# Optimization experiments

Measured on AMD Instinct MI355X. Metric: run time of the kernel, lower is better.

Reference implementation:

```python
import jax, jax.numpy as jnp
import numpy as np

TOP_K = 2


def setup_inputs() -> dict:
    key = jax.random.key(0)
    k1, k2 = jax.random.split(key)
    x = jax.random.normal(k1, (4, 4096, 2048), dtype=jnp.float32)
    W = jax.random.normal(k2, (64, 2048), dtype=jnp.float32) * (1.0 / np.sqrt(2048))
    return {"x": x, "W": W}


def reference(x, W):
    B, S, D = x.shape
    E = W.shape[0]
    # logits: [B*S, E] via linear router (no bias)
    flat = x.reshape(-1, D)
    logits = jnp.einsum('td,ed->te', flat, W)
    probs = jax.nn.softmax(logits, axis=-1)
    # eval path: top-k indices
    _, top_k_indices = jax.lax.top_k(probs, TOP_K)          # [T, K]
    # scatter 1s -> mask; scatter gathered probs -> router_probs (== probs*mask)
    router_mask = jax.nn.one_hot(top_k_indices, E, dtype=probs.dtype).sum(axis=-2)  # [T, E]
    router_probs = probs * router_mask
    # normalize (top_k > 1: gradient flows through the sum)
    router_probs = router_probs / router_probs.sum(axis=-1, keepdims=True)
    return (router_mask.reshape(B, S, E),
            top_k_indices.reshape(B, S, TOP_K),
            router_probs.reshape(B, S, E),
            probs.reshape(B, S, E))
```

## Files before the change

kernel.cpp:

```cpp
#include <hip/hip_runtime.h>
#include <math.h>


#define D_DIM 2048
#define E_DIM 64
#define NCH   (D_DIM >> 6)

typedef __bf16 bf16x8 __attribute__((ext_vector_type(8)));
typedef unsigned short us8 __attribute__((ext_vector_type(8)));
typedef float f32x4 __attribute__((ext_vector_type(4)));

static __device__ __forceinline__ unsigned short f2bf(float f) {
    unsigned int u = __float_as_uint(f);
    u += 0x7fffu + ((u >> 16) & 1u);
    return (unsigned short)(u >> 16);
}
static __device__ __forceinline__ float bf2f(unsigned short h) {
    return __uint_as_float(((unsigned int)h) << 16);
}
static __device__ __forceinline__ void split4(const float4 v, ushort4* h, ushort4* l) {
    h->x = f2bf(v.x); l->x = f2bf(v.x - bf2f(h->x));
    h->y = f2bf(v.y); l->y = f2bf(v.y - bf2f(h->y));
    h->z = f2bf(v.z); l->z = f2bf(v.z - bf2f(h->z));
    h->w = f2bf(v.w); l->w = f2bf(v.w - bf2f(h->w));
}

static __device__ __forceinline__ void gld_lds16(const void* g, void* l) {
    __builtin_amdgcn_global_load_lds(
        (const __attribute__((address_space(1))) unsigned int*)g,
        (__attribute__((address_space(3))) unsigned int*)l,
        16, 0, 0);
}

__global__ __launch_bounds__(256, 1) void convert_w(
    const float4* __restrict__ W4, unsigned short* __restrict__ WH,
    unsigned short* __restrict__ WL)
{
    int i = blockIdx.x * 256 + threadIdx.x;
    float4 v = W4[i];
    ushort4 h, l;
    split4(v, &h, &l);
    *(ushort4*)&WH[i * 4] = h;
    *(ushort4*)&WL[i * 4] = l;
}

__global__ __launch_bounds__(256, 4) void router_fused(
    const float* __restrict__ x,
    const unsigned short* __restrict__ WHg, const unsigned short* __restrict__ WLg,
    float* __restrict__ mask_out, float* __restrict__ idx_out,
    float* __restrict__ rp_out, float* __restrict__ probs_out)
{
    __shared__ __align__(16) unsigned short XH [2][16 * 64];
    __shared__ __align__(16) unsigned short XL [2][16 * 64];
    __shared__ __align__(16) unsigned short WHs[2][64 * 64];
    __shared__ __align__(16) unsigned short WLs[2][64 * 64];

    const int tid  = threadIdx.x;
    const int lane = tid & 63;
    const int wv   = tid >> 6;
    const int quad = lane >> 4;
    const int l16  = lane & 15;

    const int t0 = blockIdx.x << 4;

    f32x4 acc = {0.f, 0.f, 0.f, 0.f};

    const int we = wv * 8 + (lane >> 3);
    const int wo = lane & 7;

    const float* xg = x + (size_t)(t0 + l16) * D_DIM + wv * 16 + quad * 4;

    const int g   = wv * 4 + quad;
    const int cwb = l16 * 128 + (((g >> 1) ^ (l16 & 7)) << 4) + (g & 1) * 8;

    float4 xc = *(const float4*)(xg);
    #pragma unroll
    for (int i2 = 0; i2 < 2; ++i2) {
        int e  = i2 * 32 + we;
        int og = wo ^ (e & 7);
        gld_lds16(WHg + (size_t)e * D_DIM + og * 8, &WHs[0][(i2 * 256 + wv * 64) * 8]);
        gld_lds16(WLg + (size_t)e * D_DIM + og * 8, &WLs[0][(i2 * 256 + wv * 64) * 8]);
    }

    for (int ch = 0; ch < NCH; ++ch) {
        const int b = ch & 1;

        float4 xn;
        if (ch + 1 < NCH) xn = *(const float4*)(xg + (ch + 1) * 64);

        {
            ushort4 h, l;
            split4(xc, &h, &l);
            *(ushort4*)((char*)&XH[b][0] + cwb) = h;
            *(ushort4*)((char*)&XL[b][0] + cwb) = l;
        }

        if (ch + 1 < NCH) asm volatile("s_waitcnt vmcnt(1)" ::: "memory");
        else              asm volatile("s_waitcnt vmcnt(0)" ::: "memory");
        asm volatile("s_waitcnt lgkmcnt(0)" ::: "memory");
        __builtin_amdgcn_sched_barrier(0);
        __builtin_amdgcn_s_barrier();
        __builtin_amdgcn_sched_barrier(0);

        if (ch + 1 < NCH) {
            const int kc = (ch + 1) << 6;
            const int nb = b ^ 1;
            #pragma unroll
            for (int i2 = 0; i2 < 2; ++i2) {
                int e  = i2 * 32 + we;
                int og = wo ^ (e & 7);
                gld_lds16(WHg + (size_t)e * D_DIM + kc + og * 8,
                          &WHs[nb][(i2 * 256 + wv * 64) * 8]);
                gld_lds16(WLg + (size_t)e * D_DIM + kc + og * 8,
                          &WLs[nb][(i2 * 256 + wv * 64) * 8]);
            }
        }

        #pragma unroll
        for (int ks = 0; ks < 2; ++ks) {
            const int sr = ks * 4 + quad;
            const int ab = l16 * 128 + ((sr ^ (l16 & 7)) << 4);
            bf16x8 ah = *(const bf16x8*)((const char*)&XH[b][0] + ab);
            bf16x8 al = *(const bf16x8*)((const char*)&XL[b][0] + ab);

            const int e = wv * 16 + l16;
            const int o = ks * 4 + quad;
            const int s = e * 8 + (o ^ (e & 7));
            bf16x8 bh = *(const bf16x8*)&WHs[b][s * 8];
            bf16x8 bl = *(const bf16x8*)&WLs[b][s * 8];
            acc = __builtin_amdgcn_mfma_f32_16x16x32_bf16(ah, bh, acc, 0, 0, 0);
            acc = __builtin_amdgcn_mfma_f32_16x16x32_bf16(al, bh, acc, 0, 0, 0);
            acc = __builtin_amdgcn_mfma_f32_16x16x32_bf16(ah, bl, acc, 0, 0, 0);
        }

        if (ch + 1 < NCH) xc = xn;
    }

    float* L = (float*)&WHs[0][0];
    #pragma unroll
    for (int r = 0; r < 4; ++r)
        L[(quad * 4 + r) * 64 + wv * 16 + l16] = acc[r];
    __syncthreads();

    for (int i = 0; i < 4; ++i) {
        const int tl = wv * 4 + i;
        const int t  = t0 + tl;
        const float v = L[tl * 64 + lane];

        float bv = v; int bi = lane;
        #pragma unroll
        for (int off = 1; off < 64; off <<= 1) {
            float ov = __shfl_xor(bv, off, 64);
            int   oi = __shfl_xor(bi, off, 64);
            bool take = (ov > bv) || (ov == bv && oi < bi);
            bv = take ? ov : bv;
            bi = take ? oi : bi;
        }
        const float m = bv; const int i1 = bi;

        const float p = __expf(v - m);
        float s = p;
        #pragma unroll
        for (int off = 1; off < 64; off <<= 1) s += __shfl_xor(s, off, 64);
        const float prob = p / s;

        const float v2 = (lane == i1) ? -INFINITY : v;
        float cv = v2; int ci = lane;
        #pragma unroll
        for (int off = 1; off < 64; off <<= 1) {
            float ov = __shfl_xor(cv, off, 64);
            int   oi = __shfl_xor(ci, off, 64);
            bool take = (ov > cv) || (ov == cv && oi < ci);
            cv = take ? ov : cv;
            ci = take ? oi : ci;
        }
        const int i2 = ci;

        const float pd = __shfl(prob, i1, 64) + __shfl(prob, i2, 64);
        const bool top = (lane == i1) || (lane == i2);

        const size_t base = (size_t)t * 64 + lane;
        mask_out[base]  = top ? 1.f : 0.f;
        rp_out[base]    = top ? prob / pd : 0.f;
        probs_out[base] = prob;
        if (lane == 0) {
            idx_out[(size_t)t * 2]     = (float)i1;
            idx_out[(size_t)t * 2 + 1] = (float)i2;
        }
    }
}

extern "C" void kernel_launch(void* const* d_in, const int* in_sizes, int n_in,
                              void* d_out, int out_size, void* d_ws, size_t ws_size,
                              hipStream_t stream) {
    const float* x = (const float*)d_in[0];
    const float* W = (const float*)d_in[1];
    float* out = (float*)d_out;

    const int T  = in_sizes[0] / D_DIM;
    const int WN = in_sizes[1];

    unsigned short* WH = (unsigned short*)d_ws;
    unsigned short* WL = WH + WN;

    float* mask_out  = out;
    float* idx_out   = out + (size_t)T * E_DIM;
    float* rp_out    = idx_out + (size_t)T * 2;
    float* probs_out = rp_out + (size_t)T * E_DIM;

    convert_w<<<dim3(WN / 1024), dim3(256), 0, stream>>>((const float4*)W, WH, WL);
    router_fused<<<dim3(T / 16), dim3(256), 0, stream>>>(
        x, WH, WL, mask_out, idx_out, rp_out, probs_out);
}
```

Before: 218.3 us.

## Load W fragments directly into registers and double-buffer across unrolled chunks

The W hi/lo bf16 tiles are no longer staged through LDS with global_load_lds. Each lane now loads its MFMA B-operand fragments straight from global memory into registers. The K loop is unrolled by two, with register double buffering of both W fragments and the next x vectors, so loads for the next chunk are issued before the current chunk's MFMAs. This removes the LDS writes and reads for W and the vmcnt waits, and cuts shared memory to the x tiles only. The trade-off is more registers and uncoalesced per-lane 16-byte global loads of W that rely on L2 hits.

```diff
diff --git a/kernel.cpp b/kernel.cpp
--- a/kernel.cpp
+++ b/kernel.cpp
@@ -7,7 +7,6 @@
 #define NCH   (D_DIM >> 6)
 
 typedef __bf16 bf16x8 __attribute__((ext_vector_type(8)));
-typedef unsigned short us8 __attribute__((ext_vector_type(8)));
 typedef float f32x4 __attribute__((ext_vector_type(4)));
 
 static __device__ __forceinline__ unsigned short f2bf(float f) {
@@ -23,13 +22,6 @@
     h->y = f2bf(v.y); l->y = f2bf(v.y - bf2f(h->y));
     h->z = f2bf(v.z); l->z = f2bf(v.z - bf2f(h->z));
     h->w = f2bf(v.w); l->w = f2bf(v.w - bf2f(h->w));
-}
-
-static __device__ __forceinline__ void gld_lds16(const void* g, void* l) {
-    __builtin_amdgcn_global_load_lds(
-        (const __attribute__((address_space(1))) unsigned int*)g,
-        (__attribute__((address_space(3))) unsigned int*)l,
-        16, 0, 0);
 }
 
 __global__ __launch_bounds__(256, 1) void convert_w(
@@ -44,16 +36,24 @@
     *(ushort4*)&WL[i * 4] = l;
 }
 
+struct WR { bf16x8 h0, h1, l0, l1; };
+
+static __device__ __forceinline__ void ldwr(
+    WR& w, const unsigned short* ph, const unsigned short* pl, int q8) {
+    w.h0 = *(const bf16x8*)(ph + q8);
+    w.h1 = *(const bf16x8*)(ph + 32 + q8);
+    w.l0 = *(const bf16x8*)(pl + q8);
+    w.l1 = *(const bf16x8*)(pl + 32 + q8);
+}
+
 __global__ __launch_bounds__(256, 4) void router_fused(
     const float* __restrict__ x,
     const unsigned short* __restrict__ WHg, const unsigned short* __restrict__ WLg,
     float* __restrict__ mask_out, float* __restrict__ idx_out,
     float* __restrict__ rp_out, float* __restrict__ probs_out)
 {
-    __shared__ __align__(16) unsigned short XH [2][16 * 64];
-    __shared__ __align__(16) unsigned short XL [2][16 * 64];
-    __shared__ __align__(16) unsigned short WHs[2][64 * 64];
-    __shared__ __align__(16) unsigned short WLs[2][64 * 64];
+    __shared__ __align__(16) unsigned short XH[2][16 * 64];
+    __shared__ __align__(16) unsigned short XL[2][16 * 64];
 
     const int tid  = threadIdx.x;
     const int lane = tid & 63;
@@ -65,78 +65,77 @@
 
     f32x4 acc = {0.f, 0.f, 0.f, 0.f};
 
-    const int we = wv * 8 + (lane >> 3);
-    const int wo = lane & 7;
-
     const float* xg = x + (size_t)(t0 + l16) * D_DIM + wv * 16 + quad * 4;
-
     const int g   = wv * 4 + quad;
     const int cwb = l16 * 128 + (((g >> 1) ^ (l16 & 7)) << 4) + (g & 1) * 8;
 
-    float4 xc = *(const float4*)(xg);
-    #pragma unroll
-    for (int i2 = 0; i2 < 2; ++i2) {
-        int e  = i2 * 32 + we;
-        int og = wo ^ (e & 7);
-        gld_lds16(WHg + (size_t)e * D_DIM + og * 8, &WHs[0][(i2 * 256 + wv * 64) * 8]);
-        gld_lds16(WLg + (size_t)e * D_DIM + og * 8, &WLs[0][(i2 * 256 + wv * 64) * 8]);
+    const int e = wv * 16 + l16;
+    const unsigned short* whp = WHg + (size_t)e * D_DIM;
+    const unsigned short* wlp = WLg + (size_t)e * D_DIM;
+    const int q8 = quad * 8;
+
+    const int ab0 = l16 * 128 + ((( quad     ) ^ (l16 & 7)) << 4);
+    const int ab1 = l16 * 128 + (((4 + quad  ) ^ (l16 & 7)) << 4);
+
+#define CONVERT_WRITE(xv, b) do {                                  \
+        ushort4 _h, _l;                                            \
+        split4((xv), &_h, &_l);                                    \
+        *(ushort4*)((char*)&XH[(b)][0] + cwb) = _h;                \
+        *(ushort4*)((char*)&XL[(b)][0] + cwb) = _l;                \
+    } while (0)
+
+#define COMPUTE(b, w) do {                                                     \
+        bf16x8 _ah0 = *(const bf16x8*)((const char*)&XH[(b)][0] + ab0);        \
+        bf16x8 _al0 = *(const bf16x8*)((const char*)&XL[(b)][0] + ab0);        \
+        acc = __builtin_amdgcn_mfma_f32_16x16x32_bf16(_ah0, (w).h0, acc, 0,0,0);\
+        acc = __builtin_amdgcn_mfma_f32_16x16x32_bf16(_al0, (w).h0, acc, 0,0,0);\
+        acc = __builtin_amdgcn_mfma_f32_16x16x32_bf16(_ah0, (w).l0, acc, 0,0,0);\
+        bf16x8 _ah1 = *(const bf16x8*)((const char*)&XH[(b)][0] + ab1);        \
+        bf16x8 _al1 = *(const bf16x8*)((const char*)&XL[(b)][0] + ab1);        \
+        acc = __builtin_amdgcn_mfma_f32_16x16x32_bf16(_ah1, (w).h1, acc, 0,0,0);\
+        acc = __builtin_amdgcn_mfma_f32_16x16x32_bf16(_al1, (w).h1, acc, 0,0,0);\
+        acc = __builtin_amdgcn_mfma_f32_16x16x32_bf16(_ah1, (w).l1, acc, 0,0,0);\
+    } while (0)
+
+#define PUBLISH() do {                                   \
+        asm volatile("s_waitcnt lgkmcnt(0)" ::: "memory");\
+        __builtin_amdgcn_sched_barrier(0);               \
+        __builtin_amdgcn_s_barrier();                    \
+        __builtin_amdgcn_sched_barrier(0);               \
+    } while (0)
+
+    WR wA, wB;
+    float4 xa, xb;
+
+    {
+        float4 x0v = *(const float4*)(xg);
+        ldwr(wA, whp, wlp, q8);
+        xa = *(const float4*)(xg + 64);
+        CONVERT_WRITE(x0v, 0);
+        PUBLISH();
     }
 
-    for (int ch = 0; ch < NCH; ++ch) {
-        const int b = ch & 1;
-
-        float4 xn;
-        if (ch + 1 < NCH) xn = *(const float4*)(xg + (ch + 1) * 64);
-
-        {
-            ushort4 h, l;
-            split4(xc, &h, &l);
-            *(ushort4*)((char*)&XH[b][0] + cwb) = h;
-            *(ushort4*)((char*)&XL[b][0] + cwb) = l;
-        }
-
-        if (ch + 1 < NCH) asm volatile("s_waitcnt vmcnt(1)" ::: "memory");
-        else              asm volatile("s_waitcnt vmcnt(0)" ::: "memory");
-        asm volatile("s_waitcnt lgkmcnt(0)" ::: "memory");
-        __builtin_amdgcn_sched_barrier(0);
-        __builtin_amdgcn_s_barrier();
-        __builtin_amdgcn_sched_barrier(0);
-
+    for (int ch = 0; ch < NCH; ch += 2) {
+        if (ch + 2 < NCH) xb = *(const float4*)(xg + (ch + 2) * 64);
+        if (ch + 1 < NCH) ldwr(wB, whp + (ch + 1) * 64, wlp + (ch + 1) * 64, q8);
+        COMPUTE(ch & 1, wA);
         if (ch + 1 < NCH) {
-            const int kc = (ch + 1) << 6;
-            const int nb = b ^ 1;
-            #pragma unroll
-            for (int i2 = 0; i2 < 2; ++i2) {
-                int e  = i2 * 32 + we;
-                int og = wo ^ (e & 7);
-                gld_lds16(WHg + (size_t)e * D_DIM + kc + og * 8,
-                          &WHs[nb][(i2 * 256 + wv * 64) * 8]);
-                gld_lds16(WLg + (size_t)e * D_DIM + kc + og * 8,
-                          &WLs[nb][(i2 * 256 + wv * 64) * 8]);
-            }
-        }
-
-        #pragma unroll
-        for (int ks = 0; ks < 2; ++ks) {
-            const int sr = ks * 4 + quad;
-            const int ab = l16 * 128 + ((sr ^ (l16 & 7)) << 4);
-            bf16x8 ah = *(const bf16x8*)((const char*)&XH[b][0] + ab);
-            bf16x8 al = *(const bf16x8*)((const char*)&XL[b][0] + ab);
-
-            const int e = wv * 16 + l16;
-            const int o = ks * 4 + quad;
-            const int s = e * 8 + (o ^ (e & 7));
-            bf16x8 bh = *(const bf16x8*)&WHs[b][s * 8];
-            bf16x8 bl = *(const bf16x8*)&WLs[b][s * 8];
-            acc = __builtin_amdgcn_mfma_f32_16x16x32_bf16(ah, bh, acc, 0, 0, 0);
-            acc = __builtin_amdgcn_mfma_f32_16x16x32_bf16(al, bh, acc, 0, 0, 0);
-            acc = __builtin_amdgcn_mfma_f32_16x16x32_bf16(ah, bl, acc, 0, 0, 0);
-        }
-
-        if (ch + 1 < NCH) xc = xn;
+            CONVERT_WRITE(xa, (ch + 1) & 1);
+            PUBLISH();
+        }
+
+        const int co = ch + 1;
+        if (co + 2 < NCH) xa = *(const float4*)(xg + (co + 2) * 64);
+        if (co + 1 < NCH) ldwr(wA, whp + (co + 1) * 64, wlp + (co + 1) * 64, q8);
+        COMPUTE(co & 1, wB);
+        if (co + 1 < NCH) {
+            CONVERT_WRITE(xb, (co + 1) & 1);
+            PUBLISH();
+        }
     }
 
-    float* L = (float*)&WHs[0][0];
+    __syncthreads();
+    float* L = (float*)&XH[0][0];
     #pragma unroll
     for (int r = 0; r < 4; ++r)
         L[(quad * 4 + r) * 64 + wv * 16 + l16] = acc[r];
@@ -188,6 +187,9 @@
             idx_out[(size_t)t * 2 + 1] = (float)i2;
         }
     }
+#undef CONVERT_WRITE
+#undef COMPUTE
+#undef PUBLISH
 }
 
 extern "C" void kernel_launch(void* const* d_in, const int* in_sizes, int n_in,
```

Result: slower. 239.0 us (+9.5%).

## Stream raw fp32 x into LDS via async loads and double tile to 32 tokens

Applied to the files above, without the earlier changes.

X tiles are now loaded straight into LDS as fp32 with global_load_lds, using a 4-deep ring buffer, instead of going through registers and being split into bf16 hi/lo before storing. The split now happens after the LDS read, inside the compute loop. Each block handles 32 tokens instead of 16, so every W chunk loaded is reused across twice as many tokens, and the pipeline runs several chunks ahead. The costs are more LDS, a lower occupancy bound (launch_bounds 2 instead of 4), half as many blocks, and split arithmetic repeated by each wave in the compute path.

```diff
diff --git a/kernel.cpp b/kernel.cpp
--- a/kernel.cpp
+++ b/kernel.cpp
@@ -44,14 +44,13 @@
     *(ushort4*)&WL[i * 4] = l;
 }
 
-__global__ __launch_bounds__(256, 4) void router_fused(
+__global__ __launch_bounds__(256, 2) void router_fused(
     const float* __restrict__ x,
     const unsigned short* __restrict__ WHg, const unsigned short* __restrict__ WLg,
     float* __restrict__ mask_out, float* __restrict__ idx_out,
     float* __restrict__ rp_out, float* __restrict__ probs_out)
 {
-    __shared__ __align__(16) unsigned short XH [2][16 * 64];
-    __shared__ __align__(16) unsigned short XL [2][16 * 64];
+    __shared__ __align__(16) float          XF [4][32 * 64];
     __shared__ __align__(16) unsigned short WHs[2][64 * 64];
     __shared__ __align__(16) unsigned short WLs[2][64 * 64];
 
@@ -61,89 +60,114 @@
     const int quad = lane >> 4;
     const int l16  = lane & 15;
 
-    const int t0 = blockIdx.x << 4;
-
-    f32x4 acc = {0.f, 0.f, 0.f, 0.f};
-
-    const int we = wv * 8 + (lane >> 3);
-    const int wo = lane & 7;
-
-    const float* xg = x + (size_t)(t0 + l16) * D_DIM + wv * 16 + quad * 4;
-
-    const int g   = wv * 4 + quad;
-    const int cwb = l16 * 128 + (((g >> 1) ^ (l16 & 7)) << 4) + (g & 1) * 8;
-
-    float4 xc = *(const float4*)(xg);
+    const int t0 = blockIdx.x << 5;
+
+    f32x4 acc[2];
+    {
+        f32x4 z = {0.f, 0.f, 0.f, 0.f};
+        acc[0] = z; acc[1] = z;
+    }
+
+    const int xr0 = wv * 4 + (lane >> 4);
+    const int xc  = (lane & 15) ^ (xr0 & 15);
+    const int we0 = wv * 8 + (lane >> 3);
+    const int wo  = (lane & 7) ^ (we0 & 7);
+
+    const int e  = wv * 16 + l16;
+    const int e8 = e * 8;
+    const int ek = e & 7;
+
+#define STAGE_X(cc, xi) do {                                                   \
+        const int _kc = (cc) << 6;                                             \
+        gld_lds16(x + (size_t)(t0 + xr0) * D_DIM + _kc + xc * 4,               \
+                  &XF[xi][(wv * 64) * 4]);                                     \
+        gld_lds16(x + (size_t)(t0 + 16 + xr0) * D_DIM + _kc + xc * 4,          \
+                  &XF[xi][(256 + wv * 64) * 4]);                               \
+    } while (0)
+
+#define STAGE_W(cc, wi) do {                                                   \
+        const int _kc = (cc) << 6;                                             \
+        gld_lds16(WHg + (size_t)we0 * D_DIM + _kc + wo * 8,                    \
+                  &WHs[wi][(wv * 64) * 8]);                                    \
+        gld_lds16(WHg + (size_t)(32 + we0) * D_DIM + _kc + wo * 8,             \
+                  &WHs[wi][(256 + wv * 64) * 8]);                              \
+        gld_lds16(WLg + (size_t)we0 * D_DIM + _kc + wo * 8,                    \
+                  &WLs[wi][(wv * 64) * 8]);                                    \
+        gld_lds16(WLg + (size_t)(32 + we0) * D_DIM + _kc + wo * 8,             \
+                  &WLs[wi][(256 + wv * 64) * 8]);                              \
+    } while (0)
+
+#define COMPUTE(wb_, xb_) do {                                                 \
+        _Pragma("unroll")                                                      \
+        for (int ks = 0; ks < 2; ++ks) {                                       \
+            const int o  = ks * 4 + quad;                                      \
+            const int sW = e8 + (o ^ ek);                                      \
+            bf16x8 bh = *(const bf16x8*)&WHs[wb_][sW * 8];                     \
+            bf16x8 bl = *(const bf16x8*)&WLs[wb_][sW * 8];                     \
+            _Pragma("unroll")                                                  \
+            for (int th = 0; th < 2; ++th) {                                   \
+                const int tr = th * 16 + l16;                                  \
+                const int c0 = ks * 8 + quad * 2;                              \
+                float4 va = *(const float4*)                                   \
+                    &XF[xb_][(tr * 16 + ( c0      ^ l16)) * 4];                \
+                float4 vb = *(const float4*)                                   \
+                    &XF[xb_][(tr * 16 + ((c0 + 1) ^ l16)) * 4];                \
+                ushort4 h0, l0, h1, l1;                                        \
+                split4(va, &h0, &l0);                                          \
+                split4(vb, &h1, &l1);                                          \
+                union { us8 u; bf16x8 b; } ua, ul;                             \
+                ua.u = (us8){h0.x, h0.y, h0.z, h0.w, h1.x, h1.y, h1.z, h1.w};  \
+                ul.u = (us8){l0.x, l0.y, l0.z, l0.w, l1.x, l1.y, l1.z, l1.w};  \
+                acc[th] = __builtin_amdgcn_mfma_f32_16x16x32_bf16(             \
+                    ua.b, bh, acc[th], 0, 0, 0);                               \
+                acc[th] = __builtin_amdgcn_mfma_f32_16x16x32_bf16(             \
+                    ul.b, bh, acc[th], 0, 0, 0);                               \
+                acc[th] = __builtin_amdgcn_mfma_f32_16x16x32_bf16(             \
+                    ua.b, bl, acc[th], 0, 0, 0);                               \
+            }                                                                  \
+        }                                                                      \
+    } while (0)
+
+#define BARX() do {                                                            \
+        __builtin_amdgcn_sched_barrier(0);                                     \
+        __builtin_amdgcn_s_barrier();                                          \
+        __builtin_amdgcn_sched_barrier(0);                                     \
+    } while (0)
+
+    STAGE_X(0, 0);
+    STAGE_X(1, 1);
+    STAGE_W(0, 0);
+    STAGE_X(2, 2);
+
+    for (int ch = 0; ch <= 28; ++ch) {
+        asm volatile("s_waitcnt vmcnt(1)" ::: "memory");
+        BARX();
+        STAGE_W(ch + 1, (ch + 1) & 1);
+        STAGE_X(ch + 3, (ch + 3) & 3);
+        COMPUTE(ch & 1, ch & 3);
+    }
+    asm volatile("s_waitcnt vmcnt(1)" ::: "memory");
+    BARX();
+    STAGE_W(30, 0);
+    COMPUTE(1, 1);
+    asm volatile("s_waitcnt vmcnt(0)" ::: "memory");
+    BARX();
+    STAGE_W(31, 1);
+    COMPUTE(0, 2);
+    asm volatile("s_waitcnt vmcnt(0)" ::: "memory");
+    BARX();
+    COMPUTE(1, 3);
+
+    float* L = (float*)&XF[0][0];
     #pragma unroll
-    for (int i2 = 0; i2 < 2; ++i2) {
-        int e  = i2 * 32 + we;
-        int og = wo ^ (e & 7);
-        gld_lds16(WHg + (size_t)e * D_DIM + og * 8, &WHs[0][(i2 * 256 + wv * 64) * 8]);
-        gld_lds16(WLg + (size_t)e * D_DIM + og * 8, &WLs[0][(i2 * 256 + wv * 64) * 8]);
-    }
-
-    for (int ch = 0; ch < NCH; ++ch) {
-        const int b = ch & 1;
-
-        float4 xn;
-        if (ch + 1 < NCH) xn = *(const float4*)(xg + (ch + 1) * 64);
-
-        {
-            ushort4 h, l;
-            split4(xc, &h, &l);
-            *(ushort4*)((char*)&XH[b][0] + cwb) = h;
-            *(ushort4*)((char*)&XL[b][0] + cwb) = l;
-        }
-
-        if (ch + 1 < NCH) asm volatile("s_waitcnt vmcnt(1)" ::: "memory");
-        else              asm volatile("s_waitcnt vmcnt(0)" ::: "memory");
-        asm volatile("s_waitcnt lgkmcnt(0)" ::: "memory");
-        __builtin_amdgcn_sched_barrier(0);
-        __builtin_amdgcn_s_barrier();
-        __builtin_amdgcn_sched_barrier(0);
-
-        if (ch + 1 < NCH) {
-            const int kc = (ch + 1) << 6;
-            const int nb = b ^ 1;
-            #pragma unroll
-            for (int i2 = 0; i2 < 2; ++i2) {
-                int e  = i2 * 32 + we;
-                int og = wo ^ (e & 7);
-                gld_lds16(WHg + (size_t)e * D_DIM + kc + og * 8,
-                          &WHs[nb][(i2 * 256 + wv * 64) * 8]);
-                gld_lds16(WLg + (size_t)e * D_DIM + kc + og * 8,
-                          &WLs[nb][(i2 * 256 + wv * 64) * 8]);
-            }
-        }
-
-        #pragma unroll
-        for (int ks = 0; ks < 2; ++ks) {
-            const int sr = ks * 4 + quad;
-            const int ab = l16 * 128 + ((sr ^ (l16 & 7)) << 4);
-            bf16x8 ah = *(const bf16x8*)((const char*)&XH[b][0] + ab);
-            bf16x8 al = *(const bf16x8*)((const char*)&XL[b][0] + ab);
-
-            const int e = wv * 16 + l16;
-            const int o = ks * 4 + quad;
-            const int s = e * 8 + (o ^ (e & 7));
-            bf16x8 bh = *(const bf16x8*)&WHs[b][s * 8];
-            bf16x8 bl = *(const bf16x8*)&WLs[b][s * 8];
-            acc = __builtin_amdgcn_mfma_f32_16x16x32_bf16(ah, bh, acc, 0, 0, 0);
-            acc = __builtin_amdgcn_mfma_f32_16x16x32_bf16(al, bh, acc, 0, 0, 0);
-            acc = __builtin_amdgcn_mfma_f32_16x16x32_bf16(ah, bl, acc, 0, 0, 0);
-        }
-
-        if (ch + 1 < NCH) xc = xn;
-    }
-
-    float* L = (float*)&WHs[0][0];
-    #pragma unroll
-    for (int r = 0; r < 4; ++r)
-        L[(quad * 4 + r) * 64 + wv * 16 + l16] = acc[r];
+    for (int th = 0; th < 2; ++th)
+        #pragma unroll
+        for (int r = 0; r < 4; ++r)
+            L[(th * 16 + quad * 4 + r) * 64 + wv * 16 + l16] = acc[th][r];
     __syncthreads();
 
-    for (int i = 0; i < 4; ++i) {
-        const int tl = wv * 4 + i;
+    for (int i = 0; i < 8; ++i) {
+        const int tl = wv * 8 + i;
         const int t  = t0 + tl;
         const float v = L[tl * 64 + lane];
 
@@ -188,6 +212,10 @@
             idx_out[(size_t)t * 2 + 1] = (float)i2;
         }
     }
+#undef STAGE_X
+#undef STAGE_W
+#undef COMPUTE
+#undef BARX
 }
 
 extern "C" void kernel_launch(void* const* d_in, const int* in_sizes, int n_in,
@@ -209,6 +237,6 @@
     float* probs_out = rp_out + (size_t)T * E_DIM;
 
     convert_w<<<dim3(WN / 1024), dim3(256), 0, stream>>>((const float4*)W, WH, WL);
-    router_fused<<<dim3(T / 16), dim3(256), 0, stream>>>(
+    router_fused<<<dim3(T / 32), dim3(256), 0, stream>>>(
         x, WH, WL, mask_out, idx_out, rp_out, probs_out);
 }
```

Result: slower. 243.9 us (+11.7%).
